# Performance work log

Hardware: AMD Instinct MI355X
Metric: run time of the kernel (lower is better)

## Reference

```python
import jax, jax.numpy as jnp
import numpy as np

HEADS = 16
DIM_HEAD = 64
LN_EPS = 1e-5


def rotate_half(t):
    # '... (j d) -> ... j d' with j=2, then cat(-x2, x1)
    d = t.shape[-1] // 2
    t1, t2 = t[..., :d], t[..., d:]
    return jnp.concatenate([-t2, t1], axis=-1)


def apply_rotary_pos_emb(t, pos):
    # t: (BT, h, L, dh); pos: (L, rotate_dim)
    rd = pos.shape[-1]
    pos = pos[None, None]  # (1, 1, L, rd)
    t_rot, t_pass = t[..., :rd], t[..., rd:]
    t_rot = t_rot * jnp.cos(pos) + rotate_half(t_rot) * jnp.sin(pos)
    return jnp.concatenate([t_rot, t_pass], axis=-1)


def setup_inputs() -> dict:
    key = jax.random.key(0)
    ks = jax.random.split(key, 4)
    B, T, L, D = 2, 8, 1024, 1024
    inner = HEADS * DIM_HEAD
    x = jax.random.normal(ks[0], (B, T * L, D), dtype=jnp.float32)
    gamma = jnp.ones((D,), jnp.float32)
    beta = jnp.zeros((D,), jnp.float32)
    W_qkv = jax.random.normal(ks[1], (D, 3 * inner), jnp.float32) * (D ** -0.5)
    b_qkv = jnp.zeros((3 * inner,), jnp.float32)
    W_out = jax.random.normal(ks[2], (inner, D), jnp.float32) * (inner ** -0.5)
    # standard GPT-NeoX-style rope angles for the spatial axis, rotate_dim=32
    rot_dim = 32
    inv_freq = 1.0 / (10000.0 ** (jnp.arange(0, rot_dim, 2, dtype=jnp.float32) / rot_dim))
    freqs = jnp.arange(L, dtype=jnp.float32)[:, None] * inv_freq[None, :]  # (L, 16)
    rotary_pos_emb = jnp.concatenate([freqs, freqs], axis=-1)  # (L, 32)
    return {"x": x, "gamma": gamma, "beta": beta, "W_qkv": W_qkv,
            "b_qkv": b_qkv, "W_out": W_out, "rotary_pos_emb": rotary_pos_emb,
            "T": T, "L": L}


def reference(x, gamma, beta, W_qkv, b_qkv, W_out, rotary_pos_emb, T, L):
    B, _, D = x.shape
    h, dh = HEADS, DIM_HEAD
    scale = dh ** -0.5
    # LayerNorm
    mean = jnp.mean(x, axis=-1, keepdims=True)
    var = jnp.mean(jnp.square(x - mean), axis=-1, keepdims=True)
    xn = (x - mean) * jax.lax.rsqrt(var + LN_EPS) * gamma + beta
    # (B, T*L, D) -> (B*T, L, D)
    xr = xn.reshape(B * T, L, D)
    qkv = xr @ W_qkv + b_qkv  # (BT, L, 3*h*dh)
    q, k, v = jnp.split(qkv, 3, axis=-1)
    def to_heads(t):
        return t.reshape(B * T, L, h, dh).transpose(0, 2, 1, 3)  # (BT, h, L, dh)
    q, k, v = map(to_heads, (q, k, v))
    q = apply_rotary_pos_emb(q, rotary_pos_emb)
    k = apply_rotary_pos_emb(k, rotary_pos_emb)
    sim = jnp.einsum('bhid,bhjd->bhij', q, k) * scale
    attn = jax.nn.softmax(sim.astype(jnp.float32), axis=-1).astype(q.dtype)
    out = jnp.einsum('bhij,bhjd->bhid', attn, v)  # (BT, h, L, dh)
    out = out.transpose(0, 2, 1, 3).reshape(B * T, L, h * dh)
    out = out @ W_out  # (BT, L, D)
    return out.reshape(B, T * L, D)
```

## Files before the change

### kernel.cpp

```cpp
#include <hip/hip_runtime.h>
#include <stdint.h>

typedef short bf16x8 __attribute__((ext_vector_type(8)));
typedef float f32x4  __attribute__((ext_vector_type(4)));
typedef unsigned short u16x4 __attribute__((ext_vector_type(4)));
typedef unsigned int   u32x2 __attribute__((ext_vector_type(2)));

#define DEV __device__ __forceinline__

DEV ushort f2bf(float f){
  unsigned u = __float_as_uint(f);
  u += 0x7FFFu + ((u >> 16) & 1u);
  return (ushort)(u >> 16);
}
DEV float bf2f(ushort h){ return __uint_as_float(((unsigned)h) << 16); }

DEV void async16(const void* g, void* l){
  __builtin_amdgcn_global_load_lds((const __attribute__((address_space(1))) void*)g,
                                   (__attribute__((address_space(3))) void*)l, 16, 0, 0);
}

__global__ __launch_bounds__(256) void ln_kernel(const float* __restrict__ x,
    const float* __restrict__ gamma, const float* __restrict__ beta,
    ushort* __restrict__ xn)
{
  int row = blockIdx.x;
  int t = threadIdx.x;
  const float4* xr = (const float4*)(x + (size_t)row * 1024);
  float4 v = xr[t];
  float s  = v.x + v.y + v.z + v.w;
  float s2 = v.x*v.x + v.y*v.y + v.z*v.z + v.w*v.w;
  #pragma unroll
  for (int o = 1; o < 64; o <<= 1) { s += __shfl_xor(s, o); s2 += __shfl_xor(s2, o); }
  __shared__ float red[8];
  int lane = t & 63, wv = t >> 6;
  if (lane == 0) { red[wv] = s; red[4 + wv] = s2; }
  __syncthreads();
  s  = red[0] + red[1] + red[2] + red[3];
  s2 = red[4] + red[5] + red[6] + red[7];
  float mean = s * (1.0f / 1024.0f);
  float var  = s2 * (1.0f / 1024.0f) - mean * mean;
  float rs = rsqrtf(var + 1e-5f);
  const float4* g4 = (const float4*)gamma;
  const float4* b4 = (const float4*)beta;
  float4 g = g4[t], b = b4[t];
  u16x4 o4;
  o4[0] = f2bf((v.x - mean) * rs * g.x + b.x);
  o4[1] = f2bf((v.y - mean) * rs * g.y + b.y);
  o4[2] = f2bf((v.z - mean) * rs * g.z + b.z);
  o4[3] = f2bf((v.w - mean) * rs * g.w + b.w);
  ((u16x4*)(xn + (size_t)row * 1024))[t] = o4;
}

__global__ __launch_bounds__(256) void trans_f32_bf16(const float* __restrict__ A,
    ushort* __restrict__ At, int R, int C)
{
  __shared__ __align__(16) ushort tile[64][65];
  int c0 = blockIdx.x * 64, r0 = blockIdx.y * 64;
  int tx = threadIdx.x & 63, ty = threadIdx.x >> 6;
  #pragma unroll
  for (int i = 0; i < 64; i += 4)
    tile[ty + i][tx] = f2bf(A[(size_t)(r0 + ty + i) * C + c0 + tx]);
  __syncthreads();
  #pragma unroll
  for (int i = 0; i < 64; i += 4)
    At[(size_t)(c0 + ty + i) * R + r0 + tx] = tile[tx][ty + i];
}

template<bool OUT_BF16, bool HAS_BIAS>
__global__ __launch_bounds__(256, 2) void gemm_bt_kernel(
    const ushort* __restrict__ A, const ushort* __restrict__ Bt,
    const float* __restrict__ bias, void* __restrict__ Cout,
    int M, int N, int K)
{
  __shared__ __align__(16) ushort As[2][128 * 64];
  __shared__ __align__(16) ushort Bs[2][128 * 64];
  const int tid = threadIdx.x, lane = tid & 63, w = tid >> 6;
  const int fr = lane & 15, fg = lane >> 4;
  const int wr = w >> 1, wc = w & 1;
  const int aRow0 = blockIdx.y * 128, bCol0 = blockIdx.x * 128;
  const int srow = lane >> 3;
  const int scol = (((lane & 7) ^ srow) << 4);
  const int swz = (fr & 7) << 4;
  const size_t ldb = (size_t)K * 2;

  f32x4 acc[4][4];
  f32x4 z = {0.f, 0.f, 0.f, 0.f};
  #pragma unroll
  for (int mf = 0; mf < 4; ++mf)
    #pragma unroll
    for (int nf = 0; nf < 4; ++nf) acc[mf][nf] = z;

  auto stage = [&](int buf, int k0) {
    const char* ab = (const char*)A + (size_t)aRow0 * ldb + (size_t)k0 * 2;
    const char* bb = (const char*)Bt + (size_t)bCol0 * ldb + (size_t)k0 * 2;
    #pragma unroll
    for (int i = 0; i < 8; ++i) {
      int idx = w * 8 + i;
      if (idx < 16) {
        async16(ab + (size_t)(idx * 8 + srow) * ldb + scol, (char*)As[buf] + idx * 1024);
      } else {
        int c = idx - 16;
        async16(bb + (size_t)(c * 8 + srow) * ldb + scol, (char*)Bs[buf] + c * 1024);
      }
    }
  };

  stage(0, 0);
  __syncthreads();
  const int nk = K >> 6;
  for (int kt = 0; kt < nk; ++kt) {
    int buf = kt & 1;
    if (kt + 1 < nk) stage(buf ^ 1, (kt + 1) << 6);
    const char* as = (const char*)As[buf];
    const char* bs = (const char*)Bs[buf];
    #pragma unroll
    for (int kc = 0; kc < 2; ++kc) {
      int kb = (kc * 64 + fg * 16) ^ swz;
      bf16x8 a[4], b[4];
      #pragma unroll
      for (int mf = 0; mf < 4; ++mf)
        a[mf] = *(const bf16x8*)(as + (wr * 64 + mf * 16 + fr) * 128 + kb);
      #pragma unroll
      for (int nf = 0; nf < 4; ++nf)
        b[nf] = *(const bf16x8*)(bs + (wc * 64 + nf * 16 + fr) * 128 + kb);
      #pragma unroll
      for (int mf = 0; mf < 4; ++mf)
        #pragma unroll
        for (int nf = 0; nf < 4; ++nf)
          acc[mf][nf] = __builtin_amdgcn_mfma_f32_16x16x32_bf16(a[mf], b[nf], acc[mf][nf], 0, 0, 0);
    }
    __syncthreads();
  }
  #pragma unroll
  for (int nf = 0; nf < 4; ++nf) {
    int gc = bCol0 + wc * 64 + nf * 16 + fr;
    float bv = HAS_BIAS ? bias[gc] : 0.0f;
    #pragma unroll
    for (int mf = 0; mf < 4; ++mf) {
      int gr = aRow0 + wr * 64 + mf * 16 + fg * 4;
      #pragma unroll
      for (int r = 0; r < 4; ++r) {
        float v = acc[mf][nf][r] + bv;
        if (OUT_BF16) ((ushort*)Cout)[(size_t)(gr + r) * N + gc] = f2bf(v);
        else          ((float*)Cout)[(size_t)(gr + r) * N + gc] = v;
      }
    }
  }
}

__global__ __launch_bounds__(256) void rope_kernel(ushort* qkv, const float* __restrict__ rope)
{
  int idx = blockIdx.x * 256 + threadIdx.x;
  int i   = idx & 15;
  int h   = (idx >> 4) & 15;
  int qk  = (idx >> 8) & 1;
  int row = idx >> 9;
  int l   = row & 1023;
  size_t base = (size_t)row * 3072 + (size_t)qk * 1024 + h * 64 + i;
  float p = rope[l * 32 + i];
  float sn, cs;
  sincosf(p, &sn, &cs);
  float a = bf2f(qkv[base]), b = bf2f(qkv[base + 16]);
  qkv[base]      = f2bf(a * cs - b * sn);
  qkv[base + 16] = f2bf(b * cs + a * sn);
}

__global__ __launch_bounds__(256) void vtrans_kernel(const ushort* __restrict__ qkv,
                                                     ushort* __restrict__ vT)
{
  __shared__ __align__(16) ushort tile[64][65];
  int bh = blockIdx.x & 255, lt = blockIdx.x >> 8;
  int bt = bh >> 4, h = bh & 15;
  int tx = threadIdx.x & 63, ty = threadIdx.x >> 6;
  const ushort* src = qkv + (size_t)(bt * 1024 + lt * 64) * 3072 + 2048 + h * 64;
  #pragma unroll
  for (int i = 0; i < 64; i += 4)
    tile[ty + i][tx] = src[(size_t)(ty + i) * 3072 + tx];
  __syncthreads();
  ushort* dst = vT + (size_t)bh * 64 * 1024 + lt * 64;
  #pragma unroll
  for (int i = 0; i < 64; i += 4)
    dst[(size_t)(ty + i) * 1024 + tx] = tile[tx][ty + i];
}

__global__ __launch_bounds__(256, 2) void attn_kernel(
    const ushort* __restrict__ qkv, const ushort* __restrict__ vT,
    ushort* __restrict__ aout)
{
  __shared__ __align__(16) ushort Ks[128 * 64];
  __shared__ __align__(16) ushort Vs[64 * 128];
  __shared__ __align__(16) ushort PQ[4 * 32 * 128];
  const int tid = threadIdx.x, lane = tid & 63, w = tid >> 6;
  const int fr = lane & 15, fg = lane >> 4;
  const int bh = blockIdx.x & 255, qt = blockIdx.x >> 8;
  const int bt = bh >> 4, h = bh & 15;
  const size_t ld = 3072;
  const ushort* qbase = qkv + (size_t)bt * 1024 * ld + h * 64;
  const ushort* kbase = qbase + 1024;
  const ushort* vtb = vT + (size_t)bh * 64 * 1024;
  const int srow = lane >> 3;
  const int scol = (((lane & 7) ^ srow) << 4);
  const int swz = (fr & 7) << 4;

  #pragma unroll
  for (int i = 0; i < 4; ++i) {
    int ch = w * 4 + i;
    async16((const char*)(qbase + (size_t)(qt * 128 + ch * 8 + srow) * ld) + scol,
            (char*)PQ + ch * 1024);
  }
  __syncthreads();
  bf16x8 qfr[2][2];
  #pragma unroll
  for (int qf = 0; qf < 2; ++qf)
    #pragma unroll
    for (int kc = 0; kc < 2; ++kc) {
      int qrow = w * 32 + qf * 16 + fr;
      qfr[qf][kc] = *(const bf16x8*)((const char*)PQ + qrow * 128 +
                                     ((kc * 64 + fg * 16) ^ ((qrow & 7) << 4)));
    }

  f32x4 o[2][4];
  f32x4 z = {0.f, 0.f, 0.f, 0.f};
  #pragma unroll
  for (int a = 0; a < 2; ++a)
    #pragma unroll
    for (int b = 0; b < 4; ++b) o[a][b] = z;
  float m_[2] = {-1e30f, -1e30f}, l_[2] = {0.f, 0.f};
  ushort* Pw = PQ + w * 4096;
  const int vrow = lane >> 4;

  for (int t = 0; t < 8; ++t) {
    #pragma unroll
    for (int i = 0; i < 4; ++i) {
      int ch = w * 4 + i;
      async16((const char*)(kbase + (size_t)(t * 128 + ch * 8 + srow) * ld) + scol,
              (char*)Ks + ch * 1024);
    }
    #pragma unroll
    for (int i = 0; i < 4; ++i) {
      int ch = w * 4 + i;
      int d = ch * 4 + vrow;
      async16((const char*)(vtb + (size_t)d * 1024) + t * 256 + ((fr << 4) ^ ((d & 7) << 4)),
              (char*)Vs + ch * 1024);
    }
    __syncthreads();

    bf16x8 kf[8][2];
    #pragma unroll
    for (int kvf = 0; kvf < 8; ++kvf)
      #pragma unroll
      for (int kc = 0; kc < 2; ++kc)
        kf[kvf][kc] = *(const bf16x8*)((const char*)Ks + (kvf * 16 + fr) * 128 +
                                       ((kc * 64 + fg * 16) ^ swz));
    float alpha[2];
    #pragma unroll
    for (int qf = 0; qf < 2; ++qf) {
      f32x4 st[8];
      #pragma unroll
      for (int kvf = 0; kvf < 8; ++kvf) st[kvf] = z;
      #pragma unroll
      for (int kc = 0; kc < 2; ++kc)
        #pragma unroll
        for (int kvf = 0; kvf < 8; ++kvf)
          st[kvf] = __builtin_amdgcn_mfma_f32_16x16x32_bf16(kf[kvf][kc], qfr[qf][kc], st[kvf], 0, 0, 0);
      float mx = -1e30f;
      #pragma unroll
      for (int kvf = 0; kvf < 8; ++kvf)
        #pragma unroll
        for (int r = 0; r < 4; ++r) {
          float vv = st[kvf][r] * 0.125f;
          st[kvf][r] = vv;
          mx = fmaxf(mx, vv);
        }
      mx = fmaxf(mx, __shfl_xor(mx, 16));
      mx = fmaxf(mx, __shfl_xor(mx, 32));
      float mn = fmaxf(m_[qf], mx);
      alpha[qf] = __expf(m_[qf] - mn);
      m_[qf] = mn;
      float sum = 0.f;
      int qrow = qf * 16 + fr;
      #pragma unroll
      for (int kvf = 0; kvf < 8; ++kvf) {
        float p0 = __expf(st[kvf][0] - mn), p1 = __expf(st[kvf][1] - mn);
        float p2 = __expf(st[kvf][2] - mn), p3 = __expf(st[kvf][3] - mn);
        sum += (p0 + p1) + (p2 + p3);
        u32x2 u;
        u[0] = (unsigned)f2bf(p0) | ((unsigned)f2bf(p1) << 16);
        u[1] = (unsigned)f2bf(p2) | ((unsigned)f2bf(p3) << 16);
        *(u32x2*)((char*)Pw + qrow * 256 + (((kvf * 32 + fg * 8)) ^ swz)) = u;
      }
      sum += __shfl_xor(sum, 16);
      sum += __shfl_xor(sum, 32);
      l_[qf] = l_[qf] * alpha[qf] + sum;
    }
    #pragma unroll
    for (int of = 0; of < 2; ++of) {
      float ar[4];
      #pragma unroll
      for (int r = 0; r < 4; ++r) ar[r] = __shfl(alpha[of], fg * 4 + r);
      #pragma unroll
      for (int cf = 0; cf < 4; ++cf)
        #pragma unroll
        for (int r = 0; r < 4; ++r) o[of][cf][r] *= ar[r];
    }
    #pragma unroll
    for (int kc4 = 0; kc4 < 4; ++kc4) {
      bf16x8 pa[2];
      #pragma unroll
      for (int of = 0; of < 2; ++of)
        pa[of] = *(const bf16x8*)((const char*)Pw + (of * 16 + fr) * 256 +
                                  ((kc4 * 64 + fg * 16) ^ swz));
      #pragma unroll
      for (int cf = 0; cf < 4; ++cf) {
        bf16x8 vb = *(const bf16x8*)((const char*)Vs + (cf * 16 + fr) * 256 +
                                     ((kc4 * 64 + fg * 16) ^ swz));
        #pragma unroll
        for (int of = 0; of < 2; ++of)
          o[of][cf] = __builtin_amdgcn_mfma_f32_16x16x32_bf16(pa[of], vb, o[of][cf], 0, 0, 0);
      }
    }
    __syncthreads();
  }
  #pragma unroll
  for (int of = 0; of < 2; ++of) {
    float li[4];
    #pragma unroll
    for (int r = 0; r < 4; ++r) li[r] = 1.0f / __shfl(l_[of], fg * 4 + r);
    #pragma unroll
    for (int cf = 0; cf < 4; ++cf)
      #pragma unroll
      for (int r = 0; r < 4; ++r) {
        int grow = bt * 1024 + qt * 128 + w * 32 + of * 16 + fg * 4 + r;
        int gcol = h * 64 + cf * 16 + fr;
        aout[(size_t)grow * 1024 + gcol] = f2bf(o[of][cf][r] * li[r]);
      }
  }
}

extern "C" void kernel_launch(void* const* d_in, const int* in_sizes, int n_in,
                              void* d_out, int out_size, void* d_ws, size_t ws_size,
                              hipStream_t stream)
{
  const float* x     = (const float*)d_in[0];
  const float* gamma = (const float*)d_in[1];
  const float* beta  = (const float*)d_in[2];
  const float* Wqkv  = (const float*)d_in[3];
  const float* bqkv  = (const float*)d_in[4];
  const float* Wout  = (const float*)d_in[5];
  const float* rope  = (const float*)d_in[6];

  char* ws = (char*)d_ws;
  ushort* xn   = (ushort*)(ws + 0);
  ushort* qkvb = (ushort*)(ws + 33554432ULL);
  ushort* vT   = (ushort*)(ws + 134217728ULL);
  ushort* Wqt  = (ushort*)(ws + 167772160ULL);
  ushort* Wot  = (ushort*)(ws + 174063616ULL);
  ushort* aout = xn;

  ln_kernel<<<16384, 256, 0, stream>>>(x, gamma, beta, xn);
  trans_f32_bf16<<<dim3(48, 16), 256, 0, stream>>>(Wqkv, Wqt, 1024, 3072);
  trans_f32_bf16<<<dim3(16, 16), 256, 0, stream>>>(Wout, Wot, 1024, 1024);
  gemm_bt_kernel<true, true><<<dim3(24, 128), 256, 0, stream>>>(
      xn, Wqt, bqkv, (void*)qkvb, 16384, 3072, 1024);
  rope_kernel<<<32768, 256, 0, stream>>>(qkvb, rope);
  vtrans_kernel<<<4096, 256, 0, stream>>>(qkvb, vT);
  attn_kernel<<<2048, 256, 0, stream>>>(qkvb, vT, aout);
  gemm_bt_kernel<false, false><<<dim3(8, 128), 256, 0, stream>>>(
      aout, Wot, nullptr, d_out, 16384, 1024, 1024);
}
```

Baseline: 374.5 us.

## Fuse RoPE into QKV GEMM epilogue and double-buffer attention KV tiles

```diff
diff --git a/kernel.cpp b/kernel.cpp
--- a/kernel.cpp
+++ b/kernel.cpp
@@ -67,10 +67,22 @@
     At[(size_t)(c0 + ty + i) * R + r0 + tx] = tile[tx][ty + i];
 }
 
-template<bool OUT_BF16, bool HAS_BIAS>
+__global__ __launch_bounds__(256) void rope_tab(const float* __restrict__ rope,
+    float* __restrict__ cs, float* __restrict__ sn)
+{
+  int i = blockIdx.x * 256 + threadIdx.x;
+  int l = i >> 4, d = i & 15;
+  float p = rope[l * 32 + d];
+  float s, c;
+  sincosf(p, &s, &c);
+  cs[i] = c; sn[i] = s;
+}
+
+template<bool OUT_BF16, bool HAS_BIAS, bool ROPE>
 __global__ __launch_bounds__(256, 2) void gemm_bt_kernel(
     const ushort* __restrict__ A, const ushort* __restrict__ Bt,
     const float* __restrict__ bias, void* __restrict__ Cout,
+    const float* __restrict__ costab, const float* __restrict__ sntab,
     int M, int N, int K)
 {
   __shared__ __align__(16) ushort As[2][128 * 64];
@@ -133,37 +145,39 @@
     __syncthreads();
   }
   #pragma unroll
-  for (int nf = 0; nf < 4; ++nf) {
-    int gc = bCol0 + wc * 64 + nf * 16 + fr;
-    float bv = HAS_BIAS ? bias[gc] : 0.0f;
+  for (int pr = 0; pr < 2; ++pr) {
+    int nf0 = pr * 2, nf1 = nf0 + 1;
+    int gc0 = bCol0 + wc * 64 + nf0 * 16 + fr;
+    int gc1 = gc0 + 16;
+    float bv0 = HAS_BIAS ? bias[gc0] : 0.0f;
+    float bv1 = HAS_BIAS ? bias[gc1] : 0.0f;
+    bool rot = ROPE && (pr == 0) && (gc0 < 2048);
     #pragma unroll
     for (int mf = 0; mf < 4; ++mf) {
-      int gr = aRow0 + wr * 64 + mf * 16 + fg * 4;
+      int gr0 = aRow0 + wr * 64 + mf * 16 + fg * 4;
       #pragma unroll
       for (int r = 0; r < 4; ++r) {
-        float v = acc[mf][nf][r] + bv;
-        if (OUT_BF16) ((ushort*)Cout)[(size_t)(gr + r) * N + gc] = f2bf(v);
-        else          ((float*)Cout)[(size_t)(gr + r) * N + gc] = v;
+        int gr = gr0 + r;
+        float a = acc[mf][nf0][r] + bv0;
+        float b = acc[mf][nf1][r] + bv1;
+        if (rot) {
+          int l = gr & 1023;
+          float cs = costab[l * 16 + fr];
+          float sn = sntab[l * 16 + fr];
+          float an = fmaf(a, cs, -b * sn);
+          b = fmaf(b, cs, a * sn);
+          a = an;
+        }
+        if (OUT_BF16) {
+          ((ushort*)Cout)[(size_t)gr * N + gc0] = f2bf(a);
+          ((ushort*)Cout)[(size_t)gr * N + gc1] = f2bf(b);
+        } else {
+          ((float*)Cout)[(size_t)gr * N + gc0] = a;
+          ((float*)Cout)[(size_t)gr * N + gc1] = b;
+        }
       }
     }
   }
-}
-
-__global__ __launch_bounds__(256) void rope_kernel(ushort* qkv, const float* __restrict__ rope)
-{
-  int idx = blockIdx.x * 256 + threadIdx.x;
-  int i   = idx & 15;
-  int h   = (idx >> 4) & 15;
-  int qk  = (idx >> 8) & 1;
-  int row = idx >> 9;
-  int l   = row & 1023;
-  size_t base = (size_t)row * 3072 + (size_t)qk * 1024 + h * 64 + i;
-  float p = rope[l * 32 + i];
-  float sn, cs;
-  sincosf(p, &sn, &cs);
-  float a = bf2f(qkv[base]), b = bf2f(qkv[base + 16]);
-  qkv[base]      = f2bf(a * cs - b * sn);
-  qkv[base + 16] = f2bf(b * cs + a * sn);
 }
 
 __global__ __launch_bounds__(256) void vtrans_kernel(const ushort* __restrict__ qkv,
@@ -188,9 +202,9 @@
     const ushort* __restrict__ qkv, const ushort* __restrict__ vT,
     ushort* __restrict__ aout)
 {
-  __shared__ __align__(16) ushort Ks[128 * 64];
-  __shared__ __align__(16) ushort Vs[64 * 128];
-  __shared__ __align__(16) ushort PQ[4 * 32 * 128];
+  __shared__ __align__(16) ushort Ks[2][64 * 64];
+  __shared__ __align__(16) ushort Vs[2][64 * 64];
+  __shared__ __align__(16) ushort Ps[4][32 * 64];
   const int tid = threadIdx.x, lane = tid & 63, w = tid >> 6;
   const int fr = lane & 15, fg = lane >> 4;
   const int bh = blockIdx.x & 255, qt = blockIdx.x >> 8;
@@ -203,21 +217,13 @@
   const int scol = (((lane & 7) ^ srow) << 4);
   const int swz = (fr & 7) << 4;
 
-  #pragma unroll
-  for (int i = 0; i < 4; ++i) {
-    int ch = w * 4 + i;
-    async16((const char*)(qbase + (size_t)(qt * 128 + ch * 8 + srow) * ld) + scol,
-            (char*)PQ + ch * 1024);
-  }
-  __syncthreads();
   bf16x8 qfr[2][2];
   #pragma unroll
   for (int qf = 0; qf < 2; ++qf)
     #pragma unroll
     for (int kc = 0; kc < 2; ++kc) {
-      int qrow = w * 32 + qf * 16 + fr;
-      qfr[qf][kc] = *(const bf16x8*)((const char*)PQ + qrow * 128 +
-                                     ((kc * 64 + fg * 16) ^ ((qrow & 7) << 4)));
+      int qrow = qt * 128 + w * 32 + qf * 16 + fr;
+      qfr[qf][kc] = *(const bf16x8*)((const char*)(qbase + (size_t)qrow * ld) + kc * 64 + fg * 16);
     }
 
   f32x4 o[2][4];
@@ -227,46 +233,45 @@
     #pragma unroll
     for (int b = 0; b < 4; ++b) o[a][b] = z;
   float m_[2] = {-1e30f, -1e30f}, l_[2] = {0.f, 0.f};
-  ushort* Pw = PQ + w * 4096;
-  const int vrow = lane >> 4;
-
-  for (int t = 0; t < 8; ++t) {
-    #pragma unroll
-    for (int i = 0; i < 4; ++i) {
-      int ch = w * 4 + i;
-      async16((const char*)(kbase + (size_t)(t * 128 + ch * 8 + srow) * ld) + scol,
-              (char*)Ks + ch * 1024);
-    }
-    #pragma unroll
-    for (int i = 0; i < 4; ++i) {
-      int ch = w * 4 + i;
-      int d = ch * 4 + vrow;
-      async16((const char*)(vtb + (size_t)d * 1024) + t * 256 + ((fr << 4) ^ ((d & 7) << 4)),
-              (char*)Vs + ch * 1024);
-    }
-    __syncthreads();
-
-    bf16x8 kf[8][2];
-    #pragma unroll
-    for (int kvf = 0; kvf < 8; ++kvf)
+
+  auto stage = [&](int buf, int t) {
+    #pragma unroll
+    for (int i = 0; i < 2; ++i) {
+      int ch = w * 2 + i;
+      async16((const char*)(kbase + (size_t)(t * 64 + ch * 8 + srow) * ld) + scol,
+              (char*)Ks[buf] + ch * 1024);
+      async16((const char*)(vtb + (size_t)(ch * 8 + srow) * 1024) + t * 128 + scol,
+              (char*)Vs[buf] + ch * 1024);
+    }
+  };
+
+  stage(0, 0);
+  __syncthreads();
+  for (int t = 0; t < 16; ++t) {
+    int cur = t & 1;
+    if (t + 1 < 16) stage(cur ^ 1, t + 1);
+
+    bf16x8 kf[4][2];
+    #pragma unroll
+    for (int kvf = 0; kvf < 4; ++kvf)
       #pragma unroll
       for (int kc = 0; kc < 2; ++kc)
-        kf[kvf][kc] = *(const bf16x8*)((const char*)Ks + (kvf * 16 + fr) * 128 +
+        kf[kvf][kc] = *(const bf16x8*)((const char*)Ks[cur] + (kvf * 16 + fr) * 128 +
                                        ((kc * 64 + fg * 16) ^ swz));
     float alpha[2];
     #pragma unroll
     for (int qf = 0; qf < 2; ++qf) {
-      f32x4 st[8];
-      #pragma unroll
-      for (int kvf = 0; kvf < 8; ++kvf) st[kvf] = z;
+      f32x4 st[4];
+      #pragma unroll
+      for (int kvf = 0; kvf < 4; ++kvf) st[kvf] = z;
       #pragma unroll
       for (int kc = 0; kc < 2; ++kc)
         #pragma unroll
-        for (int kvf = 0; kvf < 8; ++kvf)
+        for (int kvf = 0; kvf < 4; ++kvf)
           st[kvf] = __builtin_amdgcn_mfma_f32_16x16x32_bf16(kf[kvf][kc], qfr[qf][kc], st[kvf], 0, 0, 0);
       float mx = -1e30f;
       #pragma unroll
-      for (int kvf = 0; kvf < 8; ++kvf)
+      for (int kvf = 0; kvf < 4; ++kvf)
         #pragma unroll
         for (int r = 0; r < 4; ++r) {
           float vv = st[kvf][r] * 0.125f;
@@ -281,14 +286,14 @@
       float sum = 0.f;
       int qrow = qf * 16 + fr;
       #pragma unroll
-      for (int kvf = 0; kvf < 8; ++kvf) {
+      for (int kvf = 0; kvf < 4; ++kvf) {
         float p0 = __expf(st[kvf][0] - mn), p1 = __expf(st[kvf][1] - mn);
         float p2 = __expf(st[kvf][2] - mn), p3 = __expf(st[kvf][3] - mn);
         sum += (p0 + p1) + (p2 + p3);
         u32x2 u;
         u[0] = (unsigned)f2bf(p0) | ((unsigned)f2bf(p1) << 16);
         u[1] = (unsigned)f2bf(p2) | ((unsigned)f2bf(p3) << 16);
-        *(u32x2*)((char*)Pw + qrow * 256 + (((kvf * 32 + fg * 8)) ^ swz)) = u;
+        *(u32x2*)((char*)Ps[w] + qrow * 128 + ((kvf * 32 + fg * 8) ^ swz)) = u;
       }
       sum += __shfl_xor(sum, 16);
       sum += __shfl_xor(sum, 32);
@@ -305,15 +310,15 @@
         for (int r = 0; r < 4; ++r) o[of][cf][r] *= ar[r];
     }
     #pragma unroll
-    for (int kc4 = 0; kc4 < 4; ++kc4) {
+    for (int kc4 = 0; kc4 < 2; ++kc4) {
       bf16x8 pa[2];
       #pragma unroll
       for (int of = 0; of < 2; ++of)
-        pa[of] = *(const bf16x8*)((const char*)Pw + (of * 16 + fr) * 256 +
+        pa[of] = *(const bf16x8*)((const char*)Ps[w] + (of * 16 + fr) * 128 +
                                   ((kc4 * 64 + fg * 16) ^ swz));
       #pragma unroll
       for (int cf = 0; cf < 4; ++cf) {
-        bf16x8 vb = *(const bf16x8*)((const char*)Vs + (cf * 16 + fr) * 256 +
+        bf16x8 vb = *(const bf16x8*)((const char*)Vs[cur] + (cf * 16 + fr) * 128 +
                                      ((kc4 * 64 + fg * 16) ^ swz));
         #pragma unroll
         for (int of = 0; of < 2; ++of)
@@ -331,9 +336,9 @@
     for (int cf = 0; cf < 4; ++cf)
       #pragma unroll
       for (int r = 0; r < 4; ++r) {
-        int grow = bt * 1024 + qt * 128 + w * 32 + of * 16 + fg * 4 + r;
-        int gcol = h * 64 + cf * 16 + fr;
-        aout[(size_t)grow * 1024 + gcol] = f2bf(o[of][cf][r] * li[r]);
+        int grow_ = bt * 1024 + qt * 128 + w * 32 + of * 16 + fg * 4 + r;
+        int gcol  = h * 64 + cf * 16 + fr;
+        aout[(size_t)grow_ * 1024 + gcol] = f2bf(o[of][cf][r] * li[r]);
       }
   }
 }
@@ -356,16 +361,18 @@
   ushort* vT   = (ushort*)(ws + 134217728ULL);
   ushort* Wqt  = (ushort*)(ws + 167772160ULL);
   ushort* Wot  = (ushort*)(ws + 174063616ULL);
+  float* costab = (float*)(ws + 176160768ULL);
+  float* sntab  = (float*)(ws + 176226304ULL);
   ushort* aout = xn;
 
   ln_kernel<<<16384, 256, 0, stream>>>(x, gamma, beta, xn);
   trans_f32_bf16<<<dim3(48, 16), 256, 0, stream>>>(Wqkv, Wqt, 1024, 3072);
   trans_f32_bf16<<<dim3(16, 16), 256, 0, stream>>>(Wout, Wot, 1024, 1024);
-  gemm_bt_kernel<true, true><<<dim3(24, 128), 256, 0, stream>>>(
-      xn, Wqt, bqkv, (void*)qkvb, 16384, 3072, 1024);
-  rope_kernel<<<32768, 256, 0, stream>>>(qkvb, rope);
+  rope_tab<<<64, 256, 0, stream>>>(rope, costab, sntab);
+  gemm_bt_kernel<true, true, true><<<dim3(24, 128), 256, 0, stream>>>(
+      xn, Wqt, bqkv, (void*)qkvb, costab, sntab, 16384, 3072, 1024);
   vtrans_kernel<<<4096, 256, 0, stream>>>(qkvb, vT);
   attn_kernel<<<2048, 256, 0, stream>>>(qkvb, vT, aout);
-  gemm_bt_kernel<false, false><<<dim3(8, 128), 256, 0, stream>>>(
-      aout, Wot, nullptr, d_out, 16384, 1024, 1024);
-}
+  gemm_bt_kernel<false, false, false><<<dim3(8, 128), 256, 0, stream>>>(
+      aout, Wot, nullptr, d_out, nullptr, nullptr, 16384, 1024, 1024);
+}
```

After: 387.4 us. 3.4% more time.
